# Optimization experiments

Measured on AMD Instinct MI355X. Metric: run time of the kernel, lower is better.

The kernel has to match this reference:

```python
import jax, jax.numpy as jnp
import numpy as np

B, N, DIM, IN_DIM, H = 8, 3136, 147, 64, 1
HD = IN_DIM // H          # per-head value/key dim = 64
MLP_HID = int(IN_DIM * 1.0)
EPS = 1e-5


def _ln(x, w, b):
    m = jnp.mean(x, axis=-1, keepdims=True)
    v = jnp.mean((x - m) ** 2, axis=-1, keepdims=True)
    return (x - m) / jnp.sqrt(v + EPS) * w + b


def setup_inputs() -> dict:
    key = jax.random.key(0)
    ks = jax.random.split(key, 12)
    r = lambda k, shp, s=0.02: (jax.random.normal(k, shp, dtype=jnp.float32) * s)
    return {
        "x": jax.random.normal(ks[0], (B, N, DIM), dtype=jnp.float32),
        "norm1_w": jnp.ones((DIM,), jnp.float32),
        "norm1_b": jnp.zeros((DIM,), jnp.float32),
        "qkv_w": r(ks[1], (3 * IN_DIM, DIM)),
        "scale": jnp.full((H,), (DIM // H) ** -0.5, dtype=jnp.float32),
        "proj_w": r(ks[2], (IN_DIM, IN_DIM)),
        "proj_b": jnp.zeros((IN_DIM,), jnp.float32),
        "norm2_w": jnp.ones((IN_DIM,), jnp.float32),
        "norm2_b": jnp.zeros((IN_DIM,), jnp.float32),
        "fc1_w": r(ks[3], (MLP_HID, IN_DIM)),
        "fc1_b": jnp.zeros((MLP_HID,), jnp.float32),
        "fc2_w": r(ks[4], (IN_DIM, MLP_HID)),
        "fc2_b": jnp.zeros((IN_DIM,), jnp.float32),
    }


def reference(x, norm1_w, norm1_b, qkv_w, scale, proj_w, proj_b,
              norm2_w, norm2_b, fc1_w, fc1_b, fc2_w, fc2_b):
    h = _ln(x, norm1_w, norm1_b)                               # [B,N,DIM]
    qkv = jnp.einsum('bnc,oc->bno', h, qkv_w)                  # [B,N,3*IN_DIM]
    qkv = qkv.reshape(B, N, 3, H, HD).transpose(2, 0, 3, 1, 4)  # [3,B,H,N,HD]
    q, k, v = qkv[0], qkv[1], qkv[2]
    # LMSA: learnable per-head scale + diagonal (self) exclusion mask
    attn = jnp.einsum('bhid,bhjd->bhij', q, k) * scale[None, :, None, None]
    eye = jnp.eye(N, dtype=bool)
    attn = jnp.where(eye[None, None], -jnp.inf, attn)
    attn = jax.nn.softmax(attn, axis=-1)
    o = jnp.einsum('bhij,bhjd->bhid', attn, v)                 # [B,H,N,HD]
    o = o.transpose(0, 2, 1, 3).reshape(B, N, IN_DIM)
    o = jnp.einsum('bnd,od->bno', o, proj_w) + proj_b
    # num_heads == 1 -> residual is v itself
    x_attn = v[:, 0] + o                                       # [B,N,IN_DIM]
    h2 = _ln(x_attn, norm2_w, norm2_b)
    h2 = jax.nn.gelu(jnp.einsum('bnd,hd->bnh', h2, fc1_w) + fc1_b,
                     approximate=False)
    h2 = jnp.einsum('bnh,oh->bno', h2, fc2_w) + fc2_b
    return x_attn + h2
```

## Files before the change

### kernel.cpp

```cpp
#include <hip/hip_runtime.h>
#include <math.h>
#include <stdint.h>

#define B_    8
#define N_    3136
#define DIM_  147
#define KP_   160
#define TOK_  (B_*N_)
#define QKV3_ 192
#define NSPLIT 4

typedef __attribute__((ext_vector_type(4)))  float f32x4;
typedef __attribute__((ext_vector_type(16))) float f32x16;
typedef __attribute__((ext_vector_type(4)))  unsigned int u32x4;
typedef __attribute__((ext_vector_type(2)))  unsigned int u32x2;
typedef __attribute__((ext_vector_type(8)))  short short8;
typedef float f32x4u __attribute__((ext_vector_type(4), aligned(4)));
typedef union { short8 s; u32x4 u; } pk8;

static __device__ __forceinline__ unsigned short f2b(float f){
  unsigned int u = __float_as_uint(f);
  u += 0x7fffu + ((u>>16)&1u);
  return (unsigned short)(u>>16);
}
static __device__ __forceinline__ unsigned int pk2(float a, float b){
  return ((unsigned int)f2b(b)<<16) | (unsigned int)f2b(a);
}
static __device__ __forceinline__ unsigned int pk2t(float a, float b){
  return (__float_as_uint(b) & 0xffff0000u) | (__float_as_uint(a)>>16);
}
static __device__ __forceinline__ float b2f(unsigned short s){
  return __uint_as_float(((unsigned int)s)<<16);
}

__global__ __launch_bounds__(256) void k_qkv(const float* __restrict__ x,
                                             const float* __restrict__ w1,
                                             const float* __restrict__ b1,
                                             const float* __restrict__ qkvw,
                                             const float* __restrict__ scale,
                                             unsigned short* __restrict__ qb,
                                             unsigned short* __restrict__ kb,
                                             unsigned short* __restrict__ vtb,
                                             unsigned short* __restrict__ vfb){
  __shared__ alignas(16) unsigned short Wb[192*168];
  unsigned short* A_ = Wb;
  unsigned short* VT = Wb;
  int tid = threadIdx.x;
  int w = tid>>6, lane = tid&63, quad = lane>>4, l16 = lane&15;
  int t0 = blockIdx.x*64;
  float sc2 = scale[0] * 1.44269504089f;

  #pragma unroll
  for(int half=0; half<2; half++){
    int g = half*32 + (tid>>3), e = tid&7;
    const float* xr = x + (size_t)(t0+g)*147;
    f32x4u xv[5];
    float s = 0.f, sq = 0.f;
    #pragma unroll
    for(int j=0;j<5;j++){
      int k = e + 8*j;
      int keff = (k > 36) ? 36 : k;
      f32x4u v = *(const f32x4u*)(xr + 4*keff);
      if(j == 4){
        v[0] = (k<=36) ? v[0] : 0.f;
        v[1] = (k<=36) ? v[1] : 0.f;
        v[2] = (k<=36) ? v[2] : 0.f;
        v[3] = (k< 36) ? v[3] : 0.f;
      }
      xv[j] = v;
      s  += (v[0]+v[1]) + (v[2]+v[3]);
      sq += (v[0]*v[0]+v[1]*v[1]) + (v[2]*v[2]+v[3]*v[3]);
    }
    s  += __shfl_xor(s,1,64);  s  += __shfl_xor(s,2,64);  s  += __shfl_xor(s,4,64);
    sq += __shfl_xor(sq,1,64); sq += __shfl_xor(sq,2,64); sq += __shfl_xor(sq,4,64);
    float mean = s*(1.f/147.f);
    float var  = sq*(1.f/147.f) - mean*mean;
    float rstd = rsqrtf(var + 1e-5f);
    #pragma unroll
    for(int j=0;j<5;j++){
      int k = e + 8*j;
      unsigned int lo = 0u, hi = 0u;
      if(k <= 36){
        int c0 = 4*k;
        int c3 = (k==36) ? 146 : c0+3;
        float y0 = (xv[j][0]-mean)*rstd*w1[c0]   + b1[c0];
        float y1 = (xv[j][1]-mean)*rstd*w1[c0+1] + b1[c0+1];
        float y2 = (xv[j][2]-mean)*rstd*w1[c0+2] + b1[c0+2];
        float y3 = (xv[j][3]-mean)*rstd*w1[c3]   + b1[c3];
        if(k == 36) y3 = 0.f;
        lo = pk2(y0,y1); hi = pk2(y2,y3);
      }
      *(u32x2*)(A_ + g*168 + 4*k) = (u32x2){lo,hi};
    }
  }
  __syncthreads();
  short8 Af[5];
  #pragma unroll
  for(int kk=0;kk<5;kk++)
    Af[kk] = *(const short8*)(A_ + (w*16+l16)*168 + kk*32 + quad*8);
  __syncthreads();
  {
    unsigned int* dst = (unsigned int*)Wb;
    #pragma unroll
    for(int rep=0; rep<15; rep++){
      int idx = rep*256 + tid;
      int row = idx/20, c = idx - row*20;
      u32x4 o = (u32x4){0u,0u,0u,0u};
      if(c < 19){
        const float* sp = qkvw + row*147 + c*8;
        f32x4u a = *(const f32x4u*)sp;
        o[0] = pk2(a[0],a[1]);
        if(c < 18){
          f32x4u bv = *(const f32x4u*)(sp+4);
          o[1] = pk2(a[2],a[3]);
          o[2] = pk2(bv[0],bv[1]);
          o[3] = pk2(bv[2],bv[3]);
        } else {
          o[1] = pk2(a[2],0.f);
        }
      }
      *(u32x4*)(dst + row*84 + c*4) = o;
    }
  }
  __syncthreads();
  f32x4 acc[12];
  #pragma unroll
  for(int i=0;i<12;i++) acc[i] = (f32x4){0.f,0.f,0.f,0.f};
  #pragma unroll
  for(int nt=0;nt<12;nt++){
    #pragma unroll
    for(int kk=0;kk<5;kk++){
      short8 Bf = *(const short8*)(Wb + (nt*16+l16)*168 + kk*32 + quad*8);
      acc[nt] = __builtin_amdgcn_mfma_f32_16x16x32_bf16(Af[kk], Bf, acc[nt], 0,0,0);
    }
  }
  #pragma unroll
  for(int nt=0;nt<12;nt++){
    int o = nt*16 + l16;
    #pragma unroll
    for(int r=0;r<4;r++){
      int tl = w*16 + quad*4 + r;
      int mg = t0 + tl;
      float val = acc[nt][r];
      if(o < 64)        qb[(size_t)mg*64 + o]        = f2b(val*sc2);
      else if(o < 128)  kb[(size_t)mg*64 + (o-64)]   = f2b(val);
      else              vfb[(size_t)mg*64 + (o-128)] = f2b(val);
    }
  }
  __syncthreads();
  #pragma unroll
  for(int nt=8;nt<12;nt++){
    int hd = (nt-8)*16 + l16;
    #pragma unroll
    for(int r=0;r<4;r++)
      VT[hd*72 + (w*16 + quad*4 + r)] = f2b(acc[nt][r]);
  }
  __syncthreads();
  {
    int b = t0 / N_, n0 = t0 - b*N_;
    const unsigned int* VT32 = (const unsigned int*)VT;
    unsigned int* vg = (unsigned int*)vtb + ((size_t)b*64)*(N_/2) + (n0>>1);
    #pragma unroll
    for(int rep=0;rep<8;rep++){
      int f = rep*256 + tid;
      int row = f>>5, c = f&31;
      vg[(size_t)row*(N_/2) + c] = VT32[row*36 + c];
    }
  }
}

__global__ __launch_bounds__(128,2) void k_attn(const unsigned short* __restrict__ qb,
                                                const unsigned short* __restrict__ kb,
                                                const unsigned short* __restrict__ vtb,
                                                unsigned short* __restrict__ Opart,
                                                float* __restrict__ lpart){
  __shared__ alignas(16) unsigned int L[4096];
  __shared__ float Lr[128];
  int tid = threadIdx.x;
  int w = tid>>6, lane = tid&63;
  int h = lane>>5, l32 = lane&31;
  int qt = blockIdx.x, sp = blockIdx.y, b = blockIdx.z;
  int q0 = qt*64;
  int kv0 = (sp*49)>>2, kv1 = ((sp+1)*49)>>2;
  int nt = kv1 - kv0;

  short8 Qf[2][4];
  {
    const unsigned short* qg = qb + ((size_t)b*N_ + q0)*64;
    #pragma unroll
    for(int qh=0;qh<2;qh++)
      #pragma unroll
      for(int kc=0;kc<4;kc++)
        Qf[qh][kc] = *(const short8*)(qg + (32*qh + l32)*64 + 16*kc + 8*h);
  }
  int sig32 = (l32 & 0x13) | ((l32&4)<<1) | ((l32&8)>>1);
  const unsigned short* kR = kb + ((size_t)b*N_ + (size_t)kv0*64 + 32*w + sig32)*64 + 8*h;
  const unsigned short* vR0 = vtb + (size_t)b*64*N_ + (size_t)l32*N_ + (size_t)kv0*64 + (4*w+h)*8;
  const unsigned short* vR1 = vR0 + (size_t)32*N_;

  short8 K0[4], K1[4], V0[4], V1[4];
#define LDK(DST, T) { const unsigned short* p_ = kR + (size_t)(T)*4096; \
    DST[0]=*(const short8*)(p_);    DST[1]=*(const short8*)(p_+16); \
    DST[2]=*(const short8*)(p_+32); DST[3]=*(const short8*)(p_+48); }
#define LDV(DST, T) { const unsigned short* p0_ = vR0 + (size_t)(T)*64; \
    const unsigned short* p1_ = vR1 + (size_t)(T)*64; \
    DST[0]=*(const short8*)(p0_); DST[1]=*(const short8*)(p0_+16); \
    DST[2]=*(const short8*)(p1_); DST[3]=*(const short8*)(p1_+16); }

  f32x16 O[2][2];
  #pragma unroll
  for(int qh=0;qh<2;qh++) for(int hdq=0;hdq<2;hdq++)
    #pragma unroll
    for(int r=0;r<16;r++) O[qh][hdq][r] = 0.f;
  float lracc[2][4];
  #pragma unroll
  for(int qh=0;qh<2;qh++)
    #pragma unroll
    for(int j=0;j<4;j++) lracc[qh][j] = 0.f;

  LDK(K0,0); LDV(V0,0);
  LDK(K1,1); LDV(V1,1);

  int i = 0;
#define TILESTEP(KC,VC) { \
    int kvt = kv0 + i; \
    _Pragma("unroll") \
    for(int qh=0;qh<2;qh++){ \
      f32x16 S; \
      _Pragma("unroll") \
      for(int r=0;r<16;r++) S[r] = 0.f; \
      _Pragma("unroll") \
      for(int kc=0;kc<4;kc++) \
        S = __builtin_amdgcn_mfma_f32_32x32x16_bf16(KC[kc], Qf[qh][kc], S, 0,0,0); \
      f32x16 E; \
      if(kvt == qt){ \
        int dref = 32*qh + l32 - 32*w - 8*h; \
        _Pragma("unroll") \
        for(int r=0;r<16;r++){ \
          int kvl = 16*((r>>3)&1) + 4*((r>>2)&1) + (r&3); \
          float pv = (kvl == dref) ? 0.f : __builtin_amdgcn_exp2f(S[r]); \
          E[r] = pv; lracc[qh][r&3] += pv; \
        } \
      } else { \
        _Pragma("unroll") \
        for(int r=0;r<16;r++){ \
          float pv = __builtin_amdgcn_exp2f(S[r]); \
          E[r] = pv; lracc[qh][r&3] += pv; \
        } \
      } \
      pk8 Pb0, Pb1; \
      Pb0.u = (u32x4){ pk2t(E[0],E[1]),   pk2t(E[2],E[3]), \
                       pk2t(E[4],E[5]),   pk2t(E[6],E[7]) }; \
      Pb1.u = (u32x4){ pk2t(E[8],E[9]),   pk2t(E[10],E[11]), \
                       pk2t(E[12],E[13]), pk2t(E[14],E[15]) }; \
      O[qh][0] = __builtin_amdgcn_mfma_f32_32x32x16_bf16(VC[0], Pb0.s, O[qh][0], 0,0,0); \
      O[qh][0] = __builtin_amdgcn_mfma_f32_32x32x16_bf16(VC[1], Pb1.s, O[qh][0], 0,0,0); \
      O[qh][1] = __builtin_amdgcn_mfma_f32_32x32x16_bf16(VC[2], Pb0.s, O[qh][1], 0,0,0); \
      O[qh][1] = __builtin_amdgcn_mfma_f32_32x32x16_bf16(VC[3], Pb1.s, O[qh][1], 0,0,0); \
    } \
    { int pf_ = i + 2; if(pf_ > nt-1) pf_ = nt-1;    \
      LDK(KC, pf_); LDV(VC, pf_); } \
    __builtin_amdgcn_sched_barrier(0); \
    i++; }

  while(i + 2 <= nt){
    TILESTEP(K0,V0);
    TILESTEP(K1,V1);
  }
  if(i < nt){ TILESTEP(K0,V0); }

#undef TILESTEP
#undef LDK
#undef LDV

  float lr[2];
  #pragma unroll
  for(int qh=0;qh<2;qh++)
    lr[qh] = (lracc[qh][0] + lracc[qh][1]) + (lracc[qh][2] + lracc[qh][3]);
  lr[0] += __shfl_xor(lr[0],32,64);
  lr[1] += __shfl_xor(lr[1],32,64);
  __syncthreads();
  if(w == 0){
    #pragma unroll
    for(int qh=0;qh<2;qh++)
      #pragma unroll
      for(int hdq=0;hdq<2;hdq++)
        #pragma unroll
        for(int r=0;r<16;r++)
          L[(qh*32 + hdq*16 + r)*64 + lane] = __float_as_uint(O[qh][hdq][r]);
    Lr[lane]      = lr[0];
    Lr[64 + lane] = lr[1];
  }
  __syncthreads();
  if(w == 1){
    #pragma unroll
    for(int qh=0;qh<2;qh++)
      #pragma unroll
      for(int hdq=0;hdq<2;hdq++)
        #pragma unroll
        for(int r=0;r<16;r++)
          O[qh][hdq][r] += __uint_as_float(L[(qh*32 + hdq*16 + r)*64 + lane]);
    float lt0 = lr[0] + Lr[lane];
    float lt1 = lr[1] + Lr[64 + lane];
    size_t lb = (size_t)sp*TOK_ + (size_t)b*N_ + q0;
    if(lane < 32){ lpart[lb + lane] = lt0; lpart[lb + 32 + lane] = lt1; }
    #pragma unroll
    for(int qh=0;qh<2;qh++){
      int q = 32*qh + l32;
      #pragma unroll
      for(int hdq=0;hdq<2;hdq++)
        #pragma unroll
        for(int k2=0;k2<8;k2++){
          int idx = 16*hdq + 4*(k2>>1) + 2*h + (k2&1);
          L[q*36 + idx] = pk2(O[qh][hdq][2*k2], O[qh][hdq][2*k2+1]);
        }
    }
    unsigned int* og = (unsigned int*)(Opart + ((size_t)sp*TOK_ + (size_t)b*N_ + q0)*64);
    #pragma unroll
    for(int rep=0;rep<8;rep++){
      int f = rep*64 + lane;
      int row = f>>3, c4 = f&7;
      *(u32x4*)(og + row*32 + c4*4) = *(const u32x4*)&L[row*36 + c4*4];
    }
  }
}

__global__ __launch_bounds__(256) void k_mlp(const unsigned short* __restrict__ Opart,
                                             const float* __restrict__ lpart,
                                             const unsigned short* __restrict__ vfb,
                                             const float* __restrict__ projw,
                                             const float* __restrict__ fc1w,
                                             const float* __restrict__ fc2w,
                                             const float* __restrict__ projb,
                                             const float* __restrict__ n2w,
                                             const float* __restrict__ n2b,
                                             const float* __restrict__ fc1b,
                                             const float* __restrict__ fc2b,
                                             float* __restrict__ out){
  __shared__ alignas(16) unsigned short Ws[3][64*72];
  __shared__ alignas(16) unsigned short Xs[64*72];
  unsigned int* Xs32 = (unsigned int*)Xs;
  int tid = threadIdx.x;
  int w = tid>>6, lane = tid&63, quad = lane>>4, l16 = lane&15;
  int t0 = blockIdx.x*64;

  {
    #pragma unroll
    for(int rep=0;rep<2;rep++){
      int f = rep*256 + tid;
      int row = f>>3, c = f&7;
      int so = (row<<6) + (c<<3);
      f32x4 a0 = *(const f32x4*)(projw + so), b0 = *(const f32x4*)(projw + so + 4);
      f32x4 a1 = *(const f32x4*)(fc1w  + so), b1v = *(const f32x4*)(fc1w  + so + 4);
      f32x4 a2 = *(const f32x4*)(fc2w  + so), b2 = *(const f32x4*)(fc2w  + so + 4);
      *(u32x4*)((unsigned int*)Ws[0] + row*36 + c*4) =
        (u32x4){pk2(a0[0],a0[1]),pk2(a0[2],a0[3]),pk2(b0[0],b0[1]),pk2(b0[2],b0[3])};
      *(u32x4*)((unsigned int*)Ws[1] + row*36 + c*4) =
        (u32x4){pk2(a1[0],a1[1]),pk2(a1[2],a1[3]),pk2(b1v[0],b1v[1]),pk2(b1v[2],b1v[3])};
      *(u32x4*)((unsigned int*)Ws[2] + row*36 + c*4) =
        (u32x4){pk2(a2[0],a2[1]),pk2(a2[2],a2[3]),pk2(b2[0],b2[1]),pk2(b2[2],b2[3])};
    }
  }
  #pragma unroll
  for(int i=0;i<2;i++){
    int f = i*256 + tid;
    int row = f>>3, c = f&7;
    float lo[4] = {0,0,0,0}, hi[4] = {0,0,0,0};
    float lsum = 0.f;
    #pragma unroll
    for(int s=0;s<NSPLIT;s++){
      u32x4 a = *((const u32x4*)(Opart + ((size_t)s*TOK_ + t0)*64) + row*8 + c);
      #pragma unroll
      for(int k=0;k<4;k++){
        lo[k] += __uint_as_float(a[k]<<16);
        hi[k] += __uint_as_float(a[k] & 0xffff0000u);
      }
      lsum += lpart[(size_t)s*TOK_ + t0 + row];
    }
    float linv = 1.f/lsum;
    u32x4 o;
    #pragma unroll
    for(int k=0;k<4;k++) o[k] = pk2(lo[k]*linv, hi[k]*linv);
    *(u32x4*)&Xs32[row*36 + c*4] = o;
  }
  __syncthreads();

  short8 Af[2];
  #pragma unroll
  for(int kk=0;kk<2;kk++)
    Af[kk] = *(const short8*)(Xs + (w*16+l16)*72 + kk*32 + quad*8);
  f32x4 acc[4];
  #pragma unroll
  for(int i=0;i<4;i++) acc[i] = (f32x4){0.f,0.f,0.f,0.f};
  #pragma unroll
  for(int jt=0;jt<4;jt++)
    #pragma unroll
    for(int kk=0;kk<2;kk++){
      short8 Bf = *(const short8*)(Ws[0] + (jt*16+l16)*72 + kk*32 + quad*8);
      acc[jt] = __builtin_amdgcn_mfma_f32_16x16x32_bf16(Af[kk], Bf, acc[jt], 0,0,0);
    }
  float xa[4][4];
  #pragma unroll
  for(int jt=0;jt<4;jt++){
    int col = jt*16 + l16;
    float pb = projb[col];
    #pragma unroll
    for(int r=0;r<4;r++){
      int tg = t0 + w*16 + quad*4 + r;
      xa[jt][r] = acc[jt][r] + pb + b2f(vfb[(size_t)tg*64 + col]);
    }
  }
  #pragma unroll
  for(int r=0;r<4;r++){
    float s = 0.f, sq = 0.f;
    #pragma unroll
    for(int jt=0;jt<4;jt++){ s += xa[jt][r]; sq += xa[jt][r]*xa[jt][r]; }
    s  += __shfl_xor(s,1,64);  s  += __shfl_xor(s,2,64);
    s  += __shfl_xor(s,4,64);  s  += __shfl_xor(s,8,64);
    sq += __shfl_xor(sq,1,64); sq += __shfl_xor(sq,2,64);
    sq += __shfl_xor(sq,4,64); sq += __shfl_xor(sq,8,64);
    float mu = s*(1.f/64.f);
    float var = sq*(1.f/64.f) - mu*mu;
    float rstd = rsqrtf(var + 1e-5f);
    #pragma unroll
    for(int jt=0;jt<4;jt++){
      int col = jt*16 + l16;
      Xs[(w*16+quad*4+r)*72 + col] = f2b((xa[jt][r]-mu)*rstd*n2w[col] + n2b[col]);
    }
  }
  #pragma unroll
  for(int kk=0;kk<2;kk++)
    Af[kk] = *(const short8*)(Xs + (w*16+l16)*72 + kk*32 + quad*8);
  f32x4 acc2[4];
  #pragma unroll
  for(int i=0;i<4;i++) acc2[i] = (f32x4){0.f,0.f,0.f,0.f};
  #pragma unroll
  for(int jt=0;jt<4;jt++)
    #pragma unroll
    for(int kk=0;kk<2;kk++){
      short8 Bf = *(const short8*)(Ws[1] + (jt*16+l16)*72 + kk*32 + quad*8);
      acc2[jt] = __builtin_amdgcn_mfma_f32_16x16x32_bf16(Af[kk], Bf, acc2[jt], 0,0,0);
    }
  #pragma unroll
  for(int jt=0;jt<4;jt++){
    int col = jt*16 + l16;
    float fb = fc1b[col];
    #pragma unroll
    for(int r=0;r<4;r++){
      float g = acc2[jt][r] + fb;
      float z = g*0.70710678118f;
      float az = fabsf(z);
      float t = 1.f/(1.f + 0.3275911f*az);
      float poly = ((((1.061405429f*t - 1.453152027f)*t + 1.421413741f)*t - 0.284496736f)*t + 0.254829592f)*t;
      float er = 1.f - poly*__builtin_amdgcn_exp2f(-az*az*1.44269504089f);
      er = (z < 0.f) ? -er : er;
      Xs[(w*16+quad*4+r)*72 + col] = f2b(0.5f*g*(1.f + er));
    }
  }
  #pragma unroll
  for(int kk=0;kk<2;kk++)
    Af[kk] = *(const short8*)(Xs + (w*16+l16)*72 + kk*32 + quad*8);
  f32x4 acc3[4];
  #pragma unroll
  for(int i=0;i<4;i++) acc3[i] = (f32x4){0.f,0.f,0.f,0.f};
  #pragma unroll
  for(int jt=0;jt<4;jt++)
    #pragma unroll
    for(int kk=0;kk<2;kk++){
      short8 Bf = *(const short8*)(Ws[2] + (jt*16+l16)*72 + kk*32 + quad*8);
      acc3[jt] = __builtin_amdgcn_mfma_f32_16x16x32_bf16(Af[kk], Bf, acc3[jt], 0,0,0);
    }
  #pragma unroll
  for(int jt=0;jt<4;jt++){
    int col = jt*16 + l16;
    float ob2 = fc2b[col];
    #pragma unroll
    for(int r=0;r<4;r++){
      int tg = t0 + w*16 + quad*4 + r;
      out[(size_t)tg*64 + col] = xa[jt][r] + acc3[jt][r] + ob2;
    }
  }
}

extern "C" void kernel_launch(void* const* d_in, const int* in_sizes, int n_in,
                              void* d_out, int out_size, void* d_ws, size_t ws_size,
                              hipStream_t stream){
  const float* x     = (const float*)d_in[0];
  const float* n1w   = (const float*)d_in[1];
  const float* n1b   = (const float*)d_in[2];
  const float* qkvw  = (const float*)d_in[3];
  const float* scale = (const float*)d_in[4];
  const float* projw = (const float*)d_in[5];
  const float* projb = (const float*)d_in[6];
  const float* n2w   = (const float*)d_in[7];
  const float* n2b   = (const float*)d_in[8];
  const float* fc1w  = (const float*)d_in[9];
  const float* fc1b  = (const float*)d_in[10];
  const float* fc2w  = (const float*)d_in[11];
  const float* fc2b  = (const float*)d_in[12];

  char* base = (char*)d_ws;
  unsigned short* qb  = (unsigned short*)(base + 0);
  unsigned short* kb  = (unsigned short*)(base + 3211264);
  unsigned short* vtb = (unsigned short*)(base + 6422528);
  unsigned short* vfb = (unsigned short*)(base + 9633792);
  unsigned short* Op  = (unsigned short*)(base + 12845056);
  float*          lp  = (float*)(base + 25690112);

  hipLaunchKernelGGL(k_qkv,  dim3(TOK_/64),    dim3(256), 0, stream,
                     x, n1w, n1b, qkvw, scale, qb, kb, vtb, vfb);
  hipLaunchKernelGGL(k_attn, dim3(49,NSPLIT,8), dim3(128), 0, stream, qb, kb, vtb, Op, lp);
  hipLaunchKernelGGL(k_mlp,  dim3(TOK_/64),    dim3(256), 0, stream, Op, lp, vfb,
                     projw, fc1w, fc2w, projb, n2w, n2b, fc1b, fc2b, (float*)d_out);
}
```

Baseline: 161.1 us.

## Stage K/V tiles through LDS with async global_load_lds double buffering

```diff
diff --git a/kernel.cpp b/kernel.cpp
--- a/kernel.cpp
+++ b/kernel.cpp
@@ -32,6 +32,11 @@
 static __device__ __forceinline__ float b2f(unsigned short s){
   return __uint_as_float(((unsigned int)s)<<16);
 }
+
+#define GLD16(gp, lp) __builtin_amdgcn_global_load_lds( \
+    reinterpret_cast<const uint32_t __attribute__((address_space(1)))*>(reinterpret_cast<uintptr_t>(gp)), \
+    reinterpret_cast<uint32_t __attribute__((address_space(3)))*>(reinterpret_cast<uintptr_t>(lp)), \
+    16, 0, 0)
 
 __global__ __launch_bounds__(256) void k_qkv(const float* __restrict__ x,
                                              const float* __restrict__ w1,
@@ -174,15 +179,16 @@
                                                 const unsigned short* __restrict__ vtb,
                                                 unsigned short* __restrict__ Opart,
                                                 float* __restrict__ lpart){
-  __shared__ alignas(16) unsigned int L[4096];
+  __shared__ alignas(16) char LB[65536];
   __shared__ float Lr[128];
   int tid = threadIdx.x;
   int w = tid>>6, lane = tid&63;
-  int h = lane>>5, l32 = lane&31;
+  int h = lane>>5, l32 = lane&31, l7 = l32&7;
   int qt = blockIdx.x, sp = blockIdx.y, b = blockIdx.z;
   int q0 = qt*64;
   int kv0 = (sp*49)>>2, kv1 = ((sp+1)*49)>>2;
-  int nt = kv1 - kv0;
+  int nfull = (kv1 - kv0)>>1;
+  int hasTail = (kv1 - kv0)&1;
 
   short8 Qf[2][4];
   {
@@ -193,19 +199,48 @@
       for(int kc=0;kc<4;kc++)
         Qf[qh][kc] = *(const short8*)(qg + (32*qh + l32)*64 + 16*kc + 8*h);
   }
-  int sig32 = (l32 & 0x13) | ((l32&4)<<1) | ((l32&8)>>1);
-  const unsigned short* kR = kb + ((size_t)b*N_ + (size_t)kv0*64 + 32*w + sig32)*64 + 8*h;
-  const unsigned short* vR0 = vtb + (size_t)b*64*N_ + (size_t)l32*N_ + (size_t)kv0*64 + (4*w+h)*8;
-  const unsigned short* vR1 = vR0 + (size_t)32*N_;
-
-  short8 K0[4], K1[4], V0[4], V1[4];
-#define LDK(DST, T) { const unsigned short* p_ = kR + (size_t)(T)*4096; \
-    DST[0]=*(const short8*)(p_);    DST[1]=*(const short8*)(p_+16); \
-    DST[2]=*(const short8*)(p_+32); DST[3]=*(const short8*)(p_+48); }
-#define LDV(DST, T) { const unsigned short* p0_ = vR0 + (size_t)(T)*64; \
-    const unsigned short* p1_ = vR1 + (size_t)(T)*64; \
-    DST[0]=*(const short8*)(p0_); DST[1]=*(const short8*)(p0_+16); \
-    DST[2]=*(const short8*)(p1_); DST[3]=*(const short8*)(p1_+16); }
+  int pl = lane>>3, cl = lane&7;
+  int pl2 = lane>>4, cl2 = lane&15;
+  int koffG[8], voffG[8];
+  #pragma unroll
+  for(int rr=0;rr<8;rr++){
+    int p = rr*8 + pl;
+    int sig = (p & 0x33) | ((p&4)<<1) | ((p&8)>>1);
+    koffG[rr] = (64*w + sig)*128 + (cl ^ (p&7))*16;
+  }
+  #pragma unroll
+  for(int rr=0;rr<8;rr++){
+    int p = rr*4 + pl2;
+    int csrc = (cl2 & 8) | ((cl2&7) ^ (p&7));
+    voffG[rr] = (32*w + p)*(N_*2) + csrc*16;
+  }
+  int koffT[4], voffT[4];
+  #pragma unroll
+  for(int rr=0;rr<4;rr++){
+    int p = rr*8 + pl;
+    int sg = (p & 0x13) | ((p&4)<<1) | ((p&8)>>1);
+    koffT[rr] = (32*w + sg)*128 + (cl ^ (p&7))*16;
+    voffT[rr] = (32*w + p)*(N_*2) + (cl ^ (p&7))*16;
+  }
+  const char* kBase = (const char*)kb + (size_t)b*N_*128;
+  const char* vBase = (const char*)vtb + (size_t)b*64*(size_t)(N_*2);
+  char* buf0 = LB;
+  char* buf1 = LB + 32768;
+
+#define STAGE128(BUFP, T) { \
+    const char* kT_ = kBase + ((size_t)(kv0)*64 + (size_t)(T)*128)*128; \
+    const char* vT_ = vBase + ((size_t)(kv0)*64 + (size_t)(T)*128)*2; \
+    _Pragma("unroll") \
+    for(int rr=0;rr<8;rr++) GLD16(kT_ + koffG[rr], (BUFP) + (2*w + (rr>>2))*4096 + (rr&3)*1024); \
+    _Pragma("unroll") \
+    for(int rr=0;rr<8;rr++) GLD16(vT_ + voffG[rr], (BUFP) + 16384 + w*8192 + rr*1024); }
+#define STAGET(BUFP) { \
+    const char* kT_ = kBase + ((size_t)(kv0)*64 + (size_t)nfull*128)*128; \
+    const char* vT_ = vBase + ((size_t)(kv0)*64 + (size_t)nfull*128)*2; \
+    _Pragma("unroll") \
+    for(int rr=0;rr<4;rr++) GLD16(kT_ + koffT[rr], (BUFP) + w*4096 + rr*1024); \
+    _Pragma("unroll") \
+    for(int rr=0;rr<4;rr++) GLD16(vT_ + voffT[rr], (BUFP) + 8192 + w*4096 + rr*1024); }
 
   f32x16 O[2][2];
   #pragma unroll
@@ -218,12 +253,11 @@
     #pragma unroll
     for(int j=0;j<4;j++) lracc[qh][j] = 0.f;
 
-  LDK(K0,0); LDV(V0,0);
-  LDK(K1,1); LDV(V1,1);
-
-  int i = 0;
-#define TILESTEP(KC,VC) { \
-    int kvt = kv0 + i; \
+#define COMPUTE64(KH, VH, VSTRIDE, VSOFF, KVT) { \
+    short8 Kf[4]; \
+    _Pragma("unroll") \
+    for(int kc=0;kc<4;kc++) \
+      Kf[kc] = *(const short8*)((KH) + l32*64 + (((2*kc+h) ^ l7)&7)*8); \
     _Pragma("unroll") \
     for(int qh=0;qh<2;qh++){ \
       f32x16 S; \
@@ -231,9 +265,9 @@
       for(int r=0;r<16;r++) S[r] = 0.f; \
       _Pragma("unroll") \
       for(int kc=0;kc<4;kc++) \
-        S = __builtin_amdgcn_mfma_f32_32x32x16_bf16(KC[kc], Qf[qh][kc], S, 0,0,0); \
+        S = __builtin_amdgcn_mfma_f32_32x32x16_bf16(Kf[kc], Qf[qh][kc], S, 0,0,0); \
       f32x16 E; \
-      if(kvt == qt){ \
+      if((KVT) == qt){ \
         int dref = 32*qh + l32 - 32*w - 8*h; \
         _Pragma("unroll") \
         for(int r=0;r<16;r++){ \
@@ -253,25 +287,55 @@
                        pk2t(E[4],E[5]),   pk2t(E[6],E[7]) }; \
       Pb1.u = (u32x4){ pk2t(E[8],E[9]),   pk2t(E[10],E[11]), \
                        pk2t(E[12],E[13]), pk2t(E[14],E[15]) }; \
-      O[qh][0] = __builtin_amdgcn_mfma_f32_32x32x16_bf16(VC[0], Pb0.s, O[qh][0], 0,0,0); \
-      O[qh][0] = __builtin_amdgcn_mfma_f32_32x32x16_bf16(VC[1], Pb1.s, O[qh][0], 0,0,0); \
-      O[qh][1] = __builtin_amdgcn_mfma_f32_32x32x16_bf16(VC[2], Pb0.s, O[qh][1], 0,0,0); \
-      O[qh][1] = __builtin_amdgcn_mfma_f32_32x32x16_bf16(VC[3], Pb1.s, O[qh][1], 0,0,0); \
-    } \
-    { int pf_ = i + 2; if(pf_ > nt-1) pf_ = nt-1;    \
-      LDK(KC, pf_); LDV(VC, pf_); } \
-    __builtin_amdgcn_sched_barrier(0); \
-    i++; }
-
-  while(i + 2 <= nt){
-    TILESTEP(K0,V0);
-    TILESTEP(K1,V1);
-  }
-  if(i < nt){ TILESTEP(K0,V0); }
-
-#undef TILESTEP
-#undef LDK
-#undef LDV
+      _Pragma("unroll") \
+      for(int hdq=0;hdq<2;hdq++){ \
+        short8 Vf0 = *(const short8*)((VH) + (32*hdq + l32)*(VSTRIDE) + (VSOFF) + (((4*w + h) ^ l7)&7)*8); \
+        short8 Vf1 = *(const short8*)((VH) + (32*hdq + l32)*(VSTRIDE) + (VSOFF) + (((4*w + 2 + h) ^ l7)&7)*8); \
+        O[qh][hdq] = __builtin_amdgcn_mfma_f32_32x32x16_bf16(Vf0, Pb0.s, O[qh][hdq], 0,0,0); \
+        O[qh][hdq] = __builtin_amdgcn_mfma_f32_32x32x16_bf16(Vf1, Pb1.s, O[qh][hdq], 0,0,0); \
+      } \
+    } }
+
+  STAGE128(buf0, 0);
+
+  for(int t=0;t<nfull;t++){
+    char* cb = (t&1) ? buf1 : buf0;
+    char* nb = (t&1) ? buf0 : buf1;
+    if(t+1 < nfull){
+      STAGE128(nb, t+1);
+      asm volatile("s_waitcnt vmcnt(16)" ::: "memory");
+    } else if(hasTail){
+      STAGET(nb);
+      asm volatile("s_waitcnt vmcnt(8)" ::: "memory");
+    } else {
+      asm volatile("s_waitcnt vmcnt(0)" ::: "memory");
+    }
+    __builtin_amdgcn_s_barrier();
+    __builtin_amdgcn_sched_barrier(0);
+
+    const unsigned short* KB_ = (const unsigned short*)cb;
+    const unsigned short* VB_ = (const unsigned short*)(cb + 16384);
+    {
+      int kvt0 = kv0 + 2*t;
+      COMPUTE64(KB_ + (0 + w)*2048, VB_, 128, 0,  kvt0);
+      COMPUTE64(KB_ + (2 + w)*2048, VB_, 128, 64, kvt0+1);
+    }
+    __builtin_amdgcn_sched_barrier(0);
+    asm volatile("" ::: "memory");
+    __builtin_amdgcn_s_barrier();
+  }
+  if(hasTail){
+    char* cb = (nfull&1) ? buf1 : buf0;
+    asm volatile("s_waitcnt vmcnt(0)" ::: "memory");
+    __builtin_amdgcn_s_barrier();
+    __builtin_amdgcn_sched_barrier(0);
+    const unsigned short* KB_ = (const unsigned short*)cb;
+    const unsigned short* VB_ = (const unsigned short*)(cb + 8192);
+    COMPUTE64(KB_ + w*2048, VB_, 64, 0, kv0 + 2*nfull);
+  }
+#undef STAGE128
+#undef STAGET
+#undef COMPUTE64
 
   float lr[2];
   #pragma unroll
@@ -279,6 +343,7 @@
     lr[qh] = (lracc[qh][0] + lracc[qh][1]) + (lracc[qh][2] + lracc[qh][3]);
   lr[0] += __shfl_xor(lr[0],32,64);
   lr[1] += __shfl_xor(lr[1],32,64);
+  unsigned int* L = (unsigned int*)LB;
   __syncthreads();
   if(w == 0){
     #pragma unroll
```

After: 159.9 us. Within noise of the previous version (-0.7%).
